# Kernel optimization log

Hardware: AMD Instinct MI355X
Metric: run time of the kernel (lower is better)

## Reference

```python
import jax, jax.numpy as jnp
import numpy as np

B = 2048          # number of graphs
NPG = 128         # nodes per graph (hard-coded by lin1 = Linear(128*hid, 1))
N = B * NPG       # total nodes = 262144
DEG = 16          # avg degree
EPG = NPG * DEG   # edges per graph
E = B * EPG       # total edges = 4194304
IN_CH = 151
HID = 64


def setup_inputs() -> dict:
    key = jax.random.key(0)
    ks = jax.random.split(key, 6)
    x = jax.random.normal(ks[0], (N, IN_CH), jnp.float32)
    # within-graph random edges: local index in [0, NPG) plus per-graph node offset
    src_loc = jax.random.randint(ks[1], (E,), 0, NPG, dtype=jnp.int32)
    dst_loc = jax.random.randint(ks[2], (E,), 0, NPG, dtype=jnp.int32)
    off = ((jnp.arange(E, dtype=jnp.int32) // EPG) * NPG)
    edge_index = jnp.stack([src_loc + off, dst_loc + off])  # [2, E] int32
    edge_weight = jax.random.uniform(ks[3], (E,), jnp.float32)
    batch = jnp.arange(N, dtype=jnp.int32) // NPG  # sorted graph ids
    W1 = jax.random.normal(ks[4], (IN_CH, HID), jnp.float32) / np.sqrt(IN_CH)
    b1 = jnp.zeros((HID,), jnp.float32)
    Wlin = jax.random.normal(ks[5], (NPG * HID, 1), jnp.float32) / np.sqrt(NPG * HID)
    blin = jnp.zeros((1,), jnp.float32)
    return {"x": x, "edge_index": edge_index, "edge_weight": edge_weight,
            "batch": batch, "W1": W1, "b1": b1, "Wlin": Wlin, "blin": blin}


def _gcn_conv(x, row, col, w, W, b, num_nodes):
    # PyG GCNConv: h = x @ W; out[col] += dinv[row]*w*dinv[col] * h[row]; out += b
    h = x @ W                                        # [N, HID]
    deg = jax.ops.segment_sum(w, col, num_segments=num_nodes)
    dinv = jnp.where(deg > 0, jax.lax.rsqrt(deg), 0.0)
    norm = dinv[row] * w * dinv[col]                 # [E+N]
    out = jax.ops.segment_sum(h[row] * norm[:, None], col, num_segments=num_nodes)
    return out + b


def reference(x, edge_index, edge_weight, batch, W1, b1, Wlin, blin):
    num_nodes = x.shape[0]
    # add self-loops with weight 1 (GCNConv default)
    sl = jnp.arange(num_nodes, dtype=edge_index.dtype)
    row = jnp.concatenate([edge_index[0], sl])
    col = jnp.concatenate([edge_index[1], sl])
    w = jnp.concatenate([edge_weight, jnp.ones((num_nodes,), x.dtype)])
    h = jax.nn.relu(_gcn_conv(x, row, col, w, W1, b1, num_nodes))  # [N, HID]
    # linearize: nodes are batch-sorted, 128 per graph -> [B, 128*HID]
    g = h.reshape(num_nodes // NPG, NPG * h.shape[1])
    return jax.nn.sigmoid(g @ Wlin + blin)  # [B, 1]
```

## Files before the change

kernel.cpp:

```cpp
#include <hip/hip_runtime.h>
#include <math.h>

#define NPG 128
#define HID 64
#define ICH 151
#define EPG 2048
#define TPB 512
#define EPT (EPG / TPB)
#define KP  160
#define HTS 136
#define ASS 132
#define AS_OFF 17408

typedef __attribute__((ext_vector_type(8))) short  short8;
typedef __attribute__((ext_vector_type(4))) float  floatx4;

static __device__ __forceinline__ unsigned short f2bf(float v) {
    unsigned u = __builtin_bit_cast(unsigned, v);
    return (unsigned short)((u + 0x7fffu + ((u >> 16) & 1u)) >> 16);
}
static __device__ __forceinline__ unsigned packbf(float a, float b) {
    return (unsigned)f2bf(a) | ((unsigned)f2bf(b) << 16);
}
static __device__ __forceinline__ short8 pack8(const float* v) {
    union { unsigned u[4]; short8 s; } r;
    r.u[0] = packbf(v[0], v[1]);
    r.u[1] = packbf(v[2], v[3]);
    r.u[2] = packbf(v[4], v[5]);
    r.u[3] = packbf(v[6], v[7]);
    return r.s;
}

__global__ __launch_bounds__(512) void gcn_prep(const float* __restrict__ W1,
                                                short* __restrict__ W1T) {
    int i = threadIdx.x + blockIdx.x * 512;
    if (i < HID * KP) {
        int ch = i / KP, k = i - ch * KP;
        W1T[i] = (short)f2bf((k < ICH) ? W1[k * HID + ch] : 0.0f);
    }
}

__global__ __launch_bounds__(TPB, 6) void gcn_fused(
    const float* __restrict__ x,
    const int*   __restrict__ erow,
    const int*   __restrict__ ecol,
    const float* __restrict__ ew,
    const short* __restrict__ W1T,
    const float* __restrict__ b1,
    const float* __restrict__ Wlin,
    const float* __restrict__ blin,
    float* __restrict__ out)
{
    __shared__ __align__(16) char smem[AS_OFF + 64 * ASS * 4];
    __shared__ float deg[NPG];
    __shared__ float red[TPB / 64];

    short* ht = (short*)smem;
    float* As = (float*)(smem + AS_OFF);

    const int t    = threadIdx.x;
    const int g    = blockIdx.x;
    const int lane = t & 63;
    const int wv   = t >> 6;
    const int c16  = lane & 15;
    const int kq   = (lane >> 4) * 8;

    if (t < NPG) deg[t] = 1.0f;

    int   ep_[EPT];
    float nw_[EPT];
    const int ebase = g * EPG;
    #pragma unroll
    for (int it = 0; it < EPT; ++it) {
        int e = ebase + t + it * TPB;
        int rl = erow[e] & (NPG - 1);
        int cl = ecol[e] & (NPG - 1);
        ep_[it] = (cl << 7) | rl;
        nw_[it] = ew[e];
    }

    short8 af[5];
    {
        const float* xr = x + (size_t)g * (NPG * ICH) + (wv * 16 + c16) * ICH;
        #pragma unroll
        for (int s = 0; s < 5; ++s) {
            float v[8];
            #pragma unroll
            for (int j = 0; j < 8; ++j) {
                int k = s * 32 + kq + j;
                v[j] = (k < ICH) ? xr[k] : 0.0f;
            }
            af[s] = pack8(v);
        }
    }

    for (int p = t; p < 64 * ASS / 4; p += TPB)
        ((floatx4*)As)[p] = (floatx4){0.0f, 0.0f, 0.0f, 0.0f};

    #pragma unroll
    for (int n = 0; n < 4; ++n) {
        floatx4 acc = {0.0f, 0.0f, 0.0f, 0.0f};
        #pragma unroll
        for (int s = 0; s < 5; ++s) {
            short8 b = *(const short8*)&W1T[(n * 16 + c16) * KP + s * 32 + kq];
            acc = __builtin_amdgcn_mfma_f32_16x16x32_bf16(af[s], b, acc, 0, 0, 0);
        }
        int col = n * 16 + c16;
        int row = wv * 16 + (lane >> 4) * 4;
        *(int2*)&ht[col * HTS + row] =
            make_int2((int)packbf(acc[0], acc[1]), (int)packbf(acc[2], acc[3]));
    }
    __syncthreads();

    #pragma unroll
    for (int it = 0; it < EPT; ++it)
        atomicAdd(&deg[ep_[it] >> 7], nw_[it]);
    __syncthreads();

    #pragma unroll
    for (int it = 0; it < EPT; ++it) {
        int rl = ep_[it] & (NPG - 1), cl = ep_[it] >> 7;
        float nrm = rsqrtf(deg[rl]) * nw_[it] * rsqrtf(deg[cl]);
        nw_[it] = nrm;
        if ((cl >> 6) == 0)
            atomicAdd(&As[(cl & 63) * ASS + rl], nrm);
    }
    if (t < 64)
        atomicAdd(&As[t * ASS + t], 1.0f / deg[t]);
    __syncthreads();

    const int mrow = (wv >> 1) * 16 + c16;
    short8 afr[4];
    #pragma unroll
    for (int ks = 0; ks < 4; ++ks) {
        const float* ap = &As[mrow * ASS + ks * 32 + kq];
        floatx4 a0 = *(const floatx4*)ap;
        floatx4 a1 = *(const floatx4*)(ap + 4);
        float v[8] = {a0[0], a0[1], a0[2], a0[3], a1[0], a1[1], a1[2], a1[3]};
        afr[ks] = pack8(v);
    }
    __syncthreads();

    for (int p = t; p < 64 * ASS / 4; p += TPB)
        ((floatx4*)As)[p] = (floatx4){0.0f, 0.0f, 0.0f, 0.0f};

    float partial = 0.0f;
    #pragma unroll
    for (int nn = 0; nn < 2; ++nn) {
        int nt2 = (wv & 1) * 2 + nn;
        floatx4 acc = {0.0f, 0.0f, 0.0f, 0.0f};
        #pragma unroll
        for (int ks = 0; ks < 4; ++ks) {
            short8 b = *(const short8*)&ht[(nt2 * 16 + c16) * HTS + ks * 32 + kq];
            acc = __builtin_amdgcn_mfma_f32_16x16x32_bf16(afr[ks], b, acc, 0, 0, 0);
        }
        int col = nt2 * 16 + c16;
        float b1v = b1[col];
        int node0 = (wv >> 1) * 16 + (lane >> 4) * 4;
        #pragma unroll
        for (int r = 0; r < 4; ++r) {
            float v = fmaxf(acc[r] + b1v, 0.0f);
            partial += v * Wlin[(node0 + r) * HID + col];
        }
    }
    __syncthreads();

    #pragma unroll
    for (int it = 0; it < EPT; ++it) {
        int cl = ep_[it] >> 7;
        if ((cl >> 6) == 1)
            atomicAdd(&As[(cl & 63) * ASS + (ep_[it] & (NPG - 1))], nw_[it]);
    }
    if (t < 64)
        atomicAdd(&As[t * ASS + 64 + t], 1.0f / deg[64 + t]);
    __syncthreads();

    #pragma unroll
    for (int ks = 0; ks < 4; ++ks) {
        const float* ap = &As[mrow * ASS + ks * 32 + kq];
        floatx4 a0 = *(const floatx4*)ap;
        floatx4 a1 = *(const floatx4*)(ap + 4);
        float v[8] = {a0[0], a0[1], a0[2], a0[3], a1[0], a1[1], a1[2], a1[3]};
        afr[ks] = pack8(v);
    }
    #pragma unroll
    for (int nn = 0; nn < 2; ++nn) {
        int nt2 = (wv & 1) * 2 + nn;
        floatx4 acc = {0.0f, 0.0f, 0.0f, 0.0f};
        #pragma unroll
        for (int ks = 0; ks < 4; ++ks) {
            short8 b = *(const short8*)&ht[(nt2 * 16 + c16) * HTS + ks * 32 + kq];
            acc = __builtin_amdgcn_mfma_f32_16x16x32_bf16(afr[ks], b, acc, 0, 0, 0);
        }
        int col = nt2 * 16 + c16;
        float b1v = b1[col];
        int node0 = 64 + (wv >> 1) * 16 + (lane >> 4) * 4;
        #pragma unroll
        for (int r = 0; r < 4; ++r) {
            float v = fmaxf(acc[r] + b1v, 0.0f);
            partial += v * Wlin[(node0 + r) * HID + col];
        }
    }

    #pragma unroll
    for (int o = 32; o > 0; o >>= 1)
        partial += __shfl_down(partial, o, 64);
    if (lane == 0) red[wv] = partial;
    __syncthreads();
    if (t == 0) {
        float tot = blin[0];
        #pragma unroll
        for (int i = 0; i < TPB / 64; ++i) tot += red[i];
        out[g] = 1.0f / (1.0f + expf(-tot));
    }
}

extern "C" void kernel_launch(void* const* d_in, const int* in_sizes, int n_in,
                              void* d_out, int out_size, void* d_ws, size_t ws_size,
                              hipStream_t stream) {
    const float* x    = (const float*)d_in[0];
    const int*   ei   = (const int*)d_in[1];
    const float* ew   = (const float*)d_in[2];
    const float* W1   = (const float*)d_in[4];
    const float* b1   = (const float*)d_in[5];
    const float* Wlin = (const float*)d_in[6];
    const float* blin = (const float*)d_in[7];
    float* out = (float*)d_out;

    const int E = in_sizes[1] / 2;
    const int B = out_size;

    short* W1T = (short*)d_ws;

    gcn_prep<<<(HID * KP + 511) / 512, 512, 0, stream>>>(W1, W1T);
    gcn_fused<<<B, TPB, 0, stream>>>(x, ei, ei + E, ew, W1T, b1, Wlin, blin, out);
}
```

Before: 100.8 us.

## Factor GCN normalization out of adjacency scatter to merge degree and edge passes

The adjacency is now accumulated with raw edge weights in the same pass as the degree atomics, and this pass overlaps the first feature matmul. The symmetric normalization moves out of the scatter: source-side dinv scales the A fragment as it is loaded, and target-side dinv scales each output row. This drops one barrier and one per-edge rsqrt pass. In exchange it adds per-fragment rsqrt work, and the second half's scatter uses raw weights, which stays correct because the same factorisation is applied there.

```diff
diff --git a/kernel.cpp b/kernel.cpp
--- a/kernel.cpp
+++ b/kernel.cpp
@@ -66,6 +66,9 @@
     const int kq   = (lane >> 4) * 8;
 
     if (t < NPG) deg[t] = 1.0f;
+    for (int p = t; p < 64 * ASS / 4; p += TPB)
+        ((floatx4*)As)[p] = (floatx4){0.0f, 0.0f, 0.0f, 0.0f};
+    __syncthreads();
 
     int   ep_[EPT];
     float nw_[EPT];
@@ -94,8 +97,15 @@
         }
     }
 
-    for (int p = t; p < 64 * ASS / 4; p += TPB)
-        ((floatx4*)As)[p] = (floatx4){0.0f, 0.0f, 0.0f, 0.0f};
+    #pragma unroll
+    for (int it = 0; it < EPT; ++it) {
+        int rl = ep_[it] & (NPG - 1), cl = ep_[it] >> 7;
+        atomicAdd(&deg[cl], nw_[it]);
+        if ((cl >> 6) == 0)
+            atomicAdd(&As[(cl & 63) * ASS + rl], nw_[it]);
+    }
+    if (t < 64)
+        atomicAdd(&As[t * ASS + t], 1.0f);
 
     #pragma unroll
     for (int n = 0; n < 4; ++n) {
@@ -112,56 +122,57 @@
     }
     __syncthreads();
 
-    #pragma unroll
-    for (int it = 0; it < EPT; ++it)
-        atomicAdd(&deg[ep_[it] >> 7], nw_[it]);
-    __syncthreads();
-
-    #pragma unroll
-    for (int it = 0; it < EPT; ++it) {
-        int rl = ep_[it] & (NPG - 1), cl = ep_[it] >> 7;
-        float nrm = rsqrtf(deg[rl]) * nw_[it] * rsqrtf(deg[cl]);
-        nw_[it] = nrm;
-        if ((cl >> 6) == 0)
-            atomicAdd(&As[(cl & 63) * ASS + rl], nrm);
-    }
-    if (t < 64)
-        atomicAdd(&As[t * ASS + t], 1.0f / deg[t]);
-    __syncthreads();
-
-    const int mrow = (wv >> 1) * 16 + c16;
-    short8 afr[4];
-    #pragma unroll
-    for (int ks = 0; ks < 4; ++ks) {
-        const float* ap = &As[mrow * ASS + ks * 32 + kq];
-        floatx4 a0 = *(const floatx4*)ap;
-        floatx4 a1 = *(const floatx4*)(ap + 4);
-        float v[8] = {a0[0], a0[1], a0[2], a0[3], a1[0], a1[1], a1[2], a1[3]};
-        afr[ks] = pack8(v);
+    const int mrow  = (wv >> 1) * 16 + c16;
+    const int rbase = (wv >> 1) * 16 + (lane >> 4) * 4;
+    float v0[2][4];
+
+    {
+        short8 afr[4];
+        #pragma unroll
+        for (int ks = 0; ks < 4; ++ks) {
+            const float* ap = &As[mrow * ASS + ks * 32 + kq];
+            floatx4 a0 = *(const floatx4*)ap;
+            floatx4 a1 = *(const floatx4*)(ap + 4);
+            floatx4 d0 = *(const floatx4*)&deg[ks * 32 + kq];
+            floatx4 d1 = *(const floatx4*)&deg[ks * 32 + kq + 4];
+            float v[8];
+            #pragma unroll
+            for (int j = 0; j < 4; ++j) {
+                v[j]     = a0[j] * rsqrtf(d0[j]);
+                v[4 + j] = a1[j] * rsqrtf(d1[j]);
+            }
+            afr[ks] = pack8(v);
+        }
+        float rs[4];
+        #pragma unroll
+        for (int r = 0; r < 4; ++r)
+            rs[r] = rsqrtf(deg[rbase + r]);
+        #pragma unroll
+        for (int nn = 0; nn < 2; ++nn) {
+            int col = ((wv & 1) * 2 + nn) * 16 + c16;
+            floatx4 acc = {0.0f, 0.0f, 0.0f, 0.0f};
+            #pragma unroll
+            for (int ks = 0; ks < 4; ++ks) {
+                short8 b = *(const short8*)&ht[col * HTS + ks * 32 + kq];
+                acc = __builtin_amdgcn_mfma_f32_16x16x32_bf16(afr[ks], b, acc, 0, 0, 0);
+            }
+            float b1v = b1[col];
+            #pragma unroll
+            for (int r = 0; r < 4; ++r)
+                v0[nn][r] = fmaxf(acc[r] * rs[r] + b1v, 0.0f);
+        }
     }
     __syncthreads();
 
     for (int p = t; p < 64 * ASS / 4; p += TPB)
         ((floatx4*)As)[p] = (floatx4){0.0f, 0.0f, 0.0f, 0.0f};
-
     float partial = 0.0f;
     #pragma unroll
     for (int nn = 0; nn < 2; ++nn) {
-        int nt2 = (wv & 1) * 2 + nn;
-        floatx4 acc = {0.0f, 0.0f, 0.0f, 0.0f};
-        #pragma unroll
-        for (int ks = 0; ks < 4; ++ks) {
-            short8 b = *(const short8*)&ht[(nt2 * 16 + c16) * HTS + ks * 32 + kq];
-            acc = __builtin_amdgcn_mfma_f32_16x16x32_bf16(afr[ks], b, acc, 0, 0, 0);
-        }
-        int col = nt2 * 16 + c16;
-        float b1v = b1[col];
-        int node0 = (wv >> 1) * 16 + (lane >> 4) * 4;
-        #pragma unroll
-        for (int r = 0; r < 4; ++r) {
-            float v = fmaxf(acc[r] + b1v, 0.0f);
-            partial += v * Wlin[(node0 + r) * HID + col];
-        }
+        int col = ((wv & 1) * 2 + nn) * 16 + c16;
+        #pragma unroll
+        for (int r = 0; r < 4; ++r)
+            partial += v0[nn][r] * Wlin[(rbase + r) * HID + col];
     }
     __syncthreads();
 
@@ -172,33 +183,45 @@
             atomicAdd(&As[(cl & 63) * ASS + (ep_[it] & (NPG - 1))], nw_[it]);
     }
     if (t < 64)
-        atomicAdd(&As[t * ASS + 64 + t], 1.0f / deg[64 + t]);
-    __syncthreads();
-
-    #pragma unroll
-    for (int ks = 0; ks < 4; ++ks) {
-        const float* ap = &As[mrow * ASS + ks * 32 + kq];
-        floatx4 a0 = *(const floatx4*)ap;
-        floatx4 a1 = *(const floatx4*)(ap + 4);
-        float v[8] = {a0[0], a0[1], a0[2], a0[3], a1[0], a1[1], a1[2], a1[3]};
-        afr[ks] = pack8(v);
-    }
-    #pragma unroll
-    for (int nn = 0; nn < 2; ++nn) {
-        int nt2 = (wv & 1) * 2 + nn;
-        floatx4 acc = {0.0f, 0.0f, 0.0f, 0.0f};
+        atomicAdd(&As[t * ASS + 64 + t], 1.0f);
+    __syncthreads();
+
+    {
+        short8 afr[4];
         #pragma unroll
         for (int ks = 0; ks < 4; ++ks) {
-            short8 b = *(const short8*)&ht[(nt2 * 16 + c16) * HTS + ks * 32 + kq];
-            acc = __builtin_amdgcn_mfma_f32_16x16x32_bf16(afr[ks], b, acc, 0, 0, 0);
-        }
-        int col = nt2 * 16 + c16;
-        float b1v = b1[col];
-        int node0 = 64 + (wv >> 1) * 16 + (lane >> 4) * 4;
-        #pragma unroll
-        for (int r = 0; r < 4; ++r) {
-            float v = fmaxf(acc[r] + b1v, 0.0f);
-            partial += v * Wlin[(node0 + r) * HID + col];
+            const float* ap = &As[mrow * ASS + ks * 32 + kq];
+            floatx4 a0 = *(const floatx4*)ap;
+            floatx4 a1 = *(const floatx4*)(ap + 4);
+            floatx4 d0 = *(const floatx4*)&deg[ks * 32 + kq];
+            floatx4 d1 = *(const floatx4*)&deg[ks * 32 + kq + 4];
+            float v[8];
+            #pragma unroll
+            for (int j = 0; j < 4; ++j) {
+                v[j]     = a0[j] * rsqrtf(d0[j]);
+                v[4 + j] = a1[j] * rsqrtf(d1[j]);
+            }
+            afr[ks] = pack8(v);
+        }
+        float rs[4];
+        #pragma unroll
+        for (int r = 0; r < 4; ++r)
+            rs[r] = rsqrtf(deg[64 + rbase + r]);
+        #pragma unroll
+        for (int nn = 0; nn < 2; ++nn) {
+            int col = ((wv & 1) * 2 + nn) * 16 + c16;
+            floatx4 acc = {0.0f, 0.0f, 0.0f, 0.0f};
+            #pragma unroll
+            for (int ks = 0; ks < 4; ++ks) {
+                short8 b = *(const short8*)&ht[col * HTS + ks * 32 + kq];
+                acc = __builtin_amdgcn_mfma_f32_16x16x32_bf16(afr[ks], b, acc, 0, 0, 0);
+            }
+            float b1v = b1[col];
+            #pragma unroll
+            for (int r = 0; r < 4; ++r) {
+                float v = fmaxf(acc[r] * rs[r] + b1v, 0.0f);
+                partial += v * Wlin[(64 + rbase + r) * HID + col];
+            }
         }
     }
 
```

After: 84.15 us. -16.5%, faster.
